# Optimization experiments

Hardware: AMD Instinct MI355X
Metric: run time of the kernel (lower is better)

## Reference

```python
import jax, jax.numpy as jnp
import numpy as np
from jax import lax

INPUT_SIZE, HIDDEN, LAYERS, OUT = 49, 32, 2, 10
B, T = 512, 1024


def _param(key, shape, fan):
    bound = 1.0 / np.sqrt(fan)
    return jax.random.uniform(key, shape, jnp.float32, -bound, bound)


def setup_inputs() -> dict:
    key = jax.random.key(0)
    ks = jax.random.split(key, 12)
    return {
        "x": jax.random.normal(ks[0], (B, T, INPUT_SIZE), jnp.float32),
        "W_ih0": _param(ks[1], (4 * HIDDEN, INPUT_SIZE), HIDDEN),
        "W_hh0": _param(ks[2], (4 * HIDDEN, HIDDEN), HIDDEN),
        "b_ih0": _param(ks[3], (4 * HIDDEN,), HIDDEN),
        "b_hh0": _param(ks[4], (4 * HIDDEN,), HIDDEN),
        "W_ih1": _param(ks[5], (4 * HIDDEN, HIDDEN), HIDDEN),
        "W_hh1": _param(ks[6], (4 * HIDDEN, HIDDEN), HIDDEN),
        "b_ih1": _param(ks[7], (4 * HIDDEN,), HIDDEN),
        "b_hh1": _param(ks[8], (4 * HIDDEN,), HIDDEN),
        "W_out": _param(ks[9], (OUT, HIDDEN), HIDDEN),
        "b_out": _param(ks[10], (OUT,), HIDDEN),
    }


def _lstm_layer(x_tbd, W_ih, W_hh, b_ih, b_hh):
    # x_tbd: [T, B, D]; PyTorch gate order i, f, g, o stacked along 4H.
    H = W_hh.shape[1]
    # Precompute input contribution for all timesteps in one GEMM.
    xg = jnp.einsum('tbd,gd->tbg', x_tbd, W_ih) + b_ih + b_hh  # [T, B, 4H]

    def step(carry, xg_t):
        h, c = carry
        gates = xg_t + h @ W_hh.T  # [B, 4H]
        i, f, g, o = jnp.split(gates, 4, axis=-1)
        i = jax.nn.sigmoid(i)
        f = jax.nn.sigmoid(f)
        g = jnp.tanh(g)
        o = jax.nn.sigmoid(o)
        c = f * c + i * g
        h = o * jnp.tanh(c)
        return (h, c), h

    Bsz = x_tbd.shape[1]
    init = (jnp.zeros((Bsz, H), x_tbd.dtype), jnp.zeros((Bsz, H), x_tbd.dtype))
    _, hs = lax.scan(step, init, xg)
    return hs  # [T, B, H]


def reference(x, W_ih0, W_hh0, b_ih0, b_hh0, W_ih1, W_hh1, b_ih1, b_hh1, W_out, b_out):
    # Eval-mode forward (inter-layer dropout disabled).
    xt = jnp.transpose(x, (1, 0, 2))  # [T, B, 49]
    h0 = _lstm_layer(xt, W_ih0, W_hh0, b_ih0, b_hh0)  # [T, B, 32]
    h1 = _lstm_layer(h0, W_ih1, W_hh1, b_ih1, b_hh1)  # [T, B, 32]
    r_out = jnp.transpose(h1, (1, 0, 2))  # [B, T, 32]
    return r_out @ W_out.T + b_out  # [B, T, 10]
```

## Files before the change

### kernel.cpp

```cpp
#include <hip/hip_runtime.h>
#include <cstddef>

#define TSTEPS 1024
#define NIN    49
#define HID    32
#define OUTD   10
#define XSTR   52
#define NGRP   256
#define RMASK  31

typedef float v2f __attribute__((ext_vector_type(2)));

template<int CTRL>
__device__ __forceinline__ float quad(float v) {
    return __int_as_float(__builtin_amdgcn_mov_dpp(__float_as_int(v), CTRL, 0xF, 0xF, true));
}
__device__ __forceinline__ float sigm(float x) {
    return __builtin_amdgcn_rcpf(1.f + __expf(-x));
}
__device__ __forceinline__ void pkfma(v2f& acc, v2f a, v2f b) {
    asm("v_pk_fma_f32 %0, %1, %2, %0" : "+v"(acc) : "v"(a), "v"(b));
}

__device__ __forceinline__ int ldacq(const int* p) {
    return __hip_atomic_load(p, __ATOMIC_ACQUIRE, __HIP_MEMORY_SCOPE_WORKGROUP);
}
__device__ __forceinline__ void pub(int* p, int v, int lane) {
    if (lane == 0)
        __hip_atomic_store(p, v, __ATOMIC_RELEASE, __HIP_MEMORY_SCOPE_WORKGROUP);
}
__device__ __forceinline__ void waitge(const int* p, int need, int& cache) {
    if (cache >= need) return;
    int c = ldacq(p);
    while (c < need) { __builtin_amdgcn_s_sleep(1); c = ldacq(p); }
    cache = c;
}

#define LOADH2(BASE, H2)                                                     \
    v2f H2[8];                                                               \
    {                                                                        \
        const float4* hp_ = (const float4*)(BASE);                           \
        const float4 a_ = hp_[0], b_ = hp_[1], c_ = hp_[2], d_ = hp_[3];     \
        H2[0] = (v2f){a_.x, a_.y}; H2[1] = (v2f){a_.z, a_.w};                \
        H2[2] = (v2f){b_.x, b_.y}; H2[3] = (v2f){b_.z, b_.w};                \
        H2[4] = (v2f){c_.x, c_.y}; H2[5] = (v2f){c_.z, c_.w};                \
        H2[6] = (v2f){d_.x, d_.y}; H2[7] = (v2f){d_.z, d_.w};                \
    }

#define DOTPK(W2, H2, S0, S1, S2, S3)                                        \
    float S0, S1, S2, S3;                                                    \
    {                                                                        \
        v2f p0 = {0.f,0.f}, p1 = {0.f,0.f}, p2 = {0.f,0.f}, p3 = {0.f,0.f}; \
        _Pragma("unroll")                                                    \
        for (int m_ = 0; m_ < 8; ++m_) {                                     \
            pkfma(p0, W2[0][m_], H2[m_]);                                    \
            pkfma(p1, W2[1][m_], H2[m_]);                                    \
            pkfma(p2, W2[2][m_], H2[m_]);                                    \
            pkfma(p3, W2[3][m_], H2[m_]);                                    \
        }                                                                    \
        S0 = p0.x + p0.y; S1 = p1.x + p1.y;                                  \
        S2 = p2.x + p2.y; S3 = p3.x + p3.y;                                  \
        S0 += quad<0xB1>(S0); S1 += quad<0xB1>(S1);                          \
        S2 += quad<0xB1>(S2); S3 += quad<0xB1>(S3);                          \
    }

__device__ __forceinline__ float gate_act(float s0, float s1, float s2, float s3,
                                          int gp, float& c) {
    const float inA = gp ? s2 + s2 : s0;
    const float inB = gp ? s3 : s1;
    const float sA = sigm(inA);
    const float sB = sigm(inB);
    const float vA = gp ? fmaf(2.f, sA, -1.f) : sA;
    const float xA = quad<0xB1>(vA);
    const float xB = quad<0xB1>(sB);
    const float fg = gp ? xB : sB;
    const float og = gp ? sB : xB;
    c = fmaf(fg, c, vA * xA);
    return og * fmaf(2.f, sigm(c + c), -1.f);
}

extern "C" __global__ void __launch_bounds__(256, 2)
lstm_amort(const float* __restrict__ x,
           const float* __restrict__ Wih0, const float* __restrict__ Whh0,
           const float* __restrict__ bih0, const float* __restrict__ bhh0,
           const float* __restrict__ Wih1, const float* __restrict__ Whh1,
           const float* __restrict__ bih1, const float* __restrict__ bhh1,
           const float* __restrict__ Wout, const float* __restrict__ bout,
           float* __restrict__ y)
{
    const int tid  = threadIdx.x;
    const int lane = tid & 63;
    const int p    = (blockIdx.x ^ (blockIdx.x >> 8)) & 1;
    const int role = (tid >> 6) ^ p;

    __shared__ __align__(16) float xs[2 * 16 * XSTR];
    __shared__ __align__(16) float xg0[32][HID][4];
    __shared__ __align__(16) float xg1[32][HID][4];
    __shared__ __align__(16) float h0r[32][HID];
    __shared__ __align__(16) float h1r[32][HID];
    __shared__ int ctr[5];

    {
        float* z0 = &h0r[0][0];
        float* z1 = &h1r[0][0];
        for (int i = tid; i < 32 * HID; i += 256) { z0[i] = 0.f; z1[i] = 0.f; }
        if (tid < 5) ctr[tid] = -1;
    }
    __syncthreads();

    const float* __restrict__ xb = x + (size_t)blockIdx.x * TSTEPS * NIN;
    float* __restrict__ yb       = y + (size_t)blockIdx.x * TSTEPS * OUTD;

    if (role == 0) {
        const int j = lane >> 1, gp = lane & 1;
        v2f wh0[4][8];
#pragma unroll
        for (int g = 0; g < 4; ++g) {
            const float* wr = Whh0 + (g * HID + j) * HID + 16 * gp;
#pragma unroll
            for (int m = 0; m < 8; ++m) wh0[g][m] = (v2f){wr[2*m], wr[2*m + 1]};
        }
        float c0 = 0.f;
        int cProd = -1, cQd = -1;
        __builtin_amdgcn_s_setprio(1);
        for (int g = 0; g < NGRP; ++g) {
            if ((g & 3) == 0) {
                waitge(&ctr[0], 4 * g + 15, cProd);
                if (g >= 8) waitge(&ctr[2], 4 * g - 17, cQd);
            }
#pragma unroll
            for (int u = 0; u < 4; ++u) {
                const int t = 4 * g + u;
                LOADH2(&h0r[(t + RMASK) & RMASK][16 * gp], hv)
                DOTPK(wh0, hv, s0, s1, s2, s3)
                const float4 xg = *(const float4*)&xg0[t & RMASK][j][0];
                const float hval = gate_act(s0 + xg.x, s1 + xg.y,
                                            s2 + xg.z, s3 + xg.w, gp, c0);
                if (gp == 0) h0r[t & RMASK][j] = hval;
            }
            pub(&ctr[1], 4 * g + 3, lane);
        }
    } else if (role == 1) {
        const int j = lane >> 1, gp = lane & 1;
        v2f wi1[4][8];
        float b1v[4];
#pragma unroll
        for (int g = 0; g < 4; ++g) {
            const float* wr = Wih1 + (g * HID + j) * HID + 16 * gp;
#pragma unroll
            for (int m = 0; m < 8; ++m) wi1[g][m] = (v2f){wr[2*m], wr[2*m + 1]};
            b1v[g] = bih1[g * HID + j] + bhh1[g * HID + j];
        }
        float wo[8], bo = 0.f;
        const int po = lane >> 2, kq = lane & 3;
        if (lane < 40) {
#pragma unroll
            for (int m = 0; m < 8; ++m) wo[m] = Wout[po * HID + kq * 8 + m];
            bo = bout[po];
        } else {
#pragma unroll
            for (int m = 0; m < 8; ++m) wo[m] = 0.f;
        }
        int cL0 = -1, cL1 = -1;
        for (int g = 0; g < NGRP; ++g) {
            if ((g & 3) == 0) {
                waitge(&ctr[1], 4 * g + 15, cL0);
                if (g >= 8) waitge(&ctr[3], 4 * g - 17, cL1);
            }
#pragma unroll
            for (int u = 0; u < 4; ++u) {
                const int t = 4 * g + u;
                LOADH2(&h0r[t & RMASK][16 * gp], hq)
                DOTPK(wi1, hq, q0, q1, q2, q3)
                if (gp == 0) {
                    float4 o;
                    o.x = q0 + b1v[0]; o.y = q1 + b1v[1];
                    o.z = q2 + b1v[2]; o.w = q3 + b1v[3];
                    *(float4*)&xg1[t & RMASK][j][0] = o;
                }
            }
            pub(&ctr[2], 4 * g + 3, lane);
            if (g >= 8) {
                const int gy = g - 8;
#pragma unroll
                for (int u = 0; u < 4; ++u) {
                    const int ty = 4 * gy + u;
                    const float* hb = &h1r[ty & RMASK][kq * 8];
                    const float4 va = *(const float4*)hb;
                    const float4 vb = *(const float4*)(hb + 4);
                    float acc = wo[0]*va.x + wo[1]*va.y + wo[2]*va.z + wo[3]*va.w
                              + wo[4]*vb.x + wo[5]*vb.y + wo[6]*vb.z + wo[7]*vb.w;
                    acc += quad<0xB1>(acc);
                    acc += quad<0x4E>(acc);
                    if (lane < 40 && kq == 0) yb[(size_t)ty * OUTD + po] = acc + bo;
                }
                pub(&ctr[4], 4 * gy + 3, lane);
            }
        }
        for (int gy = NGRP - 8; gy < NGRP; ++gy) {
            waitge(&ctr[3], 4 * gy + 3, cL1);
#pragma unroll
            for (int u = 0; u < 4; ++u) {
                const int ty = 4 * gy + u;
                const float* hb = &h1r[ty & RMASK][kq * 8];
                const float4 va = *(const float4*)hb;
                const float4 vb = *(const float4*)(hb + 4);
                float acc = wo[0]*va.x + wo[1]*va.y + wo[2]*va.z + wo[3]*va.w
                          + wo[4]*vb.x + wo[5]*vb.y + wo[6]*vb.z + wo[7]*vb.w;
                acc += quad<0xB1>(acc);
                acc += quad<0x4E>(acc);
                if (lane < 40 && kq == 0) yb[(size_t)ty * OUTD + po] = acc + bo;
            }
            pub(&ctr[4], 4 * gy + 3, lane);
        }
    } else if (role == 2) {
        const int j = lane >> 1, gp = lane & 1;
        v2f wh1[4][8];
#pragma unroll
        for (int g = 0; g < 4; ++g) {
            const float* wr = Whh1 + (g * HID + j) * HID + 16 * gp;
#pragma unroll
            for (int m = 0; m < 8; ++m) wh1[g][m] = (v2f){wr[2*m], wr[2*m + 1]};
        }
        float c1 = 0.f;
        int cQd = -1, cPrj = -1;
        __builtin_amdgcn_s_setprio(1);
        for (int g = 0; g < NGRP; ++g) {
            if ((g & 3) == 0) {
                waitge(&ctr[2], 4 * g + 15, cQd);
                if (g >= 8) waitge(&ctr[4], 4 * g - 17, cPrj);
            }
#pragma unroll
            for (int u = 0; u < 4; ++u) {
                const int t = 4 * g + u;
                LOADH2(&h1r[(t + RMASK) & RMASK][16 * gp], hv)
                DOTPK(wh1, hv, s0, s1, s2, s3)
                const float4 xg = *(const float4*)&xg1[t & RMASK][j][0];
                const float hval = gate_act(s0 + xg.x, s1 + xg.y,
                                            s2 + xg.z, s3 + xg.w, gp, c1);
                if (gp == 0) h1r[t & RMASK][j] = hval;
            }
            pub(&ctr[3], 4 * g + 3, lane);
        }
    } else {
        const int jj = lane & 31;
        const int gA = lane >> 5;
        const int gB = 2 + (lane >> 5);

        v2f wa2[24], wb2[24];
        float wa48, wb48, b0a, b0b;
        {
            const float* wra = Wih0 + (gA * HID + jj) * NIN;
            const float* wrb = Wih0 + (gB * HID + jj) * NIN;
#pragma unroll
            for (int m = 0; m < 24; ++m) {
                wa2[m] = (v2f){wra[2*m], wra[2*m + 1]};
                wb2[m] = (v2f){wrb[2*m], wrb[2*m + 1]};
            }
            wa48 = wra[48]; wb48 = wrb[48];
            b0a = bih0[gA * HID + jj] + bhh0[gA * HID + jj];
            b0b = bih0[gB * HID + jj] + bhh0[gB * HID + jj];
        }

        int laddr[13];
#pragma unroll
        for (int r = 0; r < 13; ++r) {
            const int idx = lane + r * 64;
            const int s_  = idx / NIN;
            laddr[r] = s_ * XSTR + (idx - s_ * NIN);
        }
        float xr[13];

        auto issue = [&](int cn) {
            const float* src = xb + (size_t)cn * 16 * NIN;
#pragma unroll
            for (int r = 0; r < 12; ++r) xr[r] = src[lane + r * 64];
            if (lane < 16) xr[12] = src[lane + 768];
        };
        auto drain = [&](int cn) {
            float* dst = &xs[(cn & 1) * (16 * XSTR)];
#pragma unroll
            for (int r = 0; r < 12; ++r) dst[laddr[r]] = xr[r];
            if (lane < 16) dst[laddr[12]] = xr[12];
        };
        auto pdot = [&](int t) {
            const float* xp = &xs[((t >> 4) & 1) * (16 * XSTR) + (t & 15) * XSTR];
            const float4* x4 = (const float4*)xp;
            v2f aA0 = (v2f){b0a, 0.f}, aA1 = (v2f){0.f, 0.f};
            v2f aB0 = (v2f){b0b, 0.f}, aB1 = (v2f){0.f, 0.f};
#pragma unroll
            for (int u = 0; u < 12; ++u) {
                const float4 xv = x4[u];
                const v2f xlo = (v2f){xv.x, xv.y};
                const v2f xhi = (v2f){xv.z, xv.w};
                pkfma(aA0, wa2[2*u],     xlo);
                pkfma(aA1, wa2[2*u + 1], xhi);
                pkfma(aB0, wb2[2*u],     xlo);
                pkfma(aB1, wb2[2*u + 1], xhi);
            }
            const float x48 = xp[48];
            const float a0 = fmaf(wa48, x48, (aA0.x + aA0.y) + (aA1.x + aA1.y));
            const float a2 = fmaf(wb48, x48, (aB0.x + aB0.y) + (aB1.x + aB1.y));
            xg0[t & RMASK][jj][gA] = a0;
            xg0[t & RMASK][jj][gB] = a2;
        };

        issue(0);
        drain(0);

        int cL0 = -1;
        for (int g = 0; g < NGRP; ++g) {
            if ((g & 3) == 0 && g >= 8)
                waitge(&ctr[1], 4 * g - 17, cL0);
            const int cn = (g >> 2) + 1;
            if ((g & 3) == 0 && cn < 64) issue(cn);
            pdot(4 * g); pdot(4 * g + 1); pdot(4 * g + 2); pdot(4 * g + 3);
            if ((g & 3) == 2 && cn < 64) drain(cn);
            pub(&ctr[0], 4 * g + 3, lane);
        }
    }
}

extern "C" void kernel_launch(void* const* d_in, const int* in_sizes, int n_in,
                              void* d_out, int out_size, void* d_ws, size_t ws_size,
                              hipStream_t stream) {
    (void)in_sizes; (void)n_in; (void)d_ws; (void)ws_size; (void)out_size;
    const float* x    = (const float*)d_in[0];
    const float* Wih0 = (const float*)d_in[1];
    const float* Whh0 = (const float*)d_in[2];
    const float* bih0 = (const float*)d_in[3];
    const float* bhh0 = (const float*)d_in[4];
    const float* Wih1 = (const float*)d_in[5];
    const float* Whh1 = (const float*)d_in[6];
    const float* bih1 = (const float*)d_in[7];
    const float* bhh1 = (const float*)d_in[8];
    const float* Wout = (const float*)d_in[9];
    const float* bout = (const float*)d_in[10];
    float* y = (float*)d_out;

    lstm_amort<<<dim3(512), dim3(256), 0, stream>>>(
        x, Wih0, Whh0, bih0, bhh0, Wih1, Whh1, bih1, bhh1, Wout, bout, y);
}
```

Baseline: 395.5 us.

## Pack two batch sequences per workgroup and shrink ring buffers to sixteen steps

Each 512-thread workgroup now runs two independent sequences, each with its own four role wavefronts and its own counters, instead of one sequence per 256-thread block. The LDS ring buffers shrink from 32 to 16 timesteps and the producer/consumer waits tighten, so wavefronts poll every two groups instead of four. The goal is to cut LDS per sequence and change how wavefronts are co-scheduled on a CU. The cost is less slack between pipeline stages, more frequent synchronisation, and a launch bound that forces one block per CU.

```diff
diff --git a/kernel.cpp b/kernel.cpp
--- a/kernel.cpp
+++ b/kernel.cpp
@@ -7,7 +7,8 @@
 #define OUTD   10
 #define XSTR   52
 #define NGRP   256
-#define RMASK  31
+#define RMASK  15
+#define NB     2
 
 typedef float v2f __attribute__((ext_vector_type(2)));
 
@@ -79,8 +80,8 @@
     return og * fmaf(2.f, sigm(c + c), -1.f);
 }
 
-extern "C" __global__ void __launch_bounds__(256, 2)
-lstm_amort(const float* __restrict__ x,
+extern "C" __global__ void __launch_bounds__(512, 1)
+lstm_pair8(const float* __restrict__ x,
            const float* __restrict__ Wih0, const float* __restrict__ Whh0,
            const float* __restrict__ bih0, const float* __restrict__ bhh0,
            const float* __restrict__ Wih1, const float* __restrict__ Whh1,
@@ -90,26 +91,28 @@
 {
     const int tid  = threadIdx.x;
     const int lane = tid & 63;
-    const int p    = (blockIdx.x ^ (blockIdx.x >> 8)) & 1;
-    const int role = (tid >> 6) ^ p;
-
-    __shared__ __align__(16) float xs[2 * 16 * XSTR];
-    __shared__ __align__(16) float xg0[32][HID][4];
-    __shared__ __align__(16) float xg1[32][HID][4];
-    __shared__ __align__(16) float h0r[32][HID];
-    __shared__ __align__(16) float h1r[32][HID];
-    __shared__ int ctr[5];
+    const int w    = tid >> 6;
+    const int bi   = w >> 2;
+    const int role = (w & 3) ^ bi;
+
+    __shared__ __align__(16) float xs[NB][2 * 16 * XSTR];
+    __shared__ __align__(16) float xg0[NB][16][HID][4];
+    __shared__ __align__(16) float xg1[NB][16][HID][4];
+    __shared__ __align__(16) float h0r[NB][16][HID];
+    __shared__ __align__(16) float h1r[NB][16][HID];
+    __shared__ int ctr[NB][5];
 
     {
-        float* z0 = &h0r[0][0];
-        float* z1 = &h1r[0][0];
-        for (int i = tid; i < 32 * HID; i += 256) { z0[i] = 0.f; z1[i] = 0.f; }
-        if (tid < 5) ctr[tid] = -1;
+        float* z0 = &h0r[0][0][0];
+        float* z1 = &h1r[0][0][0];
+        for (int i = tid; i < NB * 16 * HID; i += 512) { z0[i] = 0.f; z1[i] = 0.f; }
+        if (tid < NB * 5) ctr[tid / 5][tid % 5] = -1;
     }
     __syncthreads();
 
-    const float* __restrict__ xb = x + (size_t)blockIdx.x * TSTEPS * NIN;
-    float* __restrict__ yb       = y + (size_t)blockIdx.x * TSTEPS * OUTD;
+    const float* __restrict__ xb = x + ((size_t)blockIdx.x * NB + bi) * TSTEPS * NIN;
+    float* __restrict__ yb       = y + ((size_t)blockIdx.x * NB + bi) * TSTEPS * OUTD;
+    int* cr = &ctr[bi][0];
 
     if (role == 0) {
         const int j = lane >> 1, gp = lane & 1;
@@ -124,21 +127,21 @@
         int cProd = -1, cQd = -1;
         __builtin_amdgcn_s_setprio(1);
         for (int g = 0; g < NGRP; ++g) {
-            if ((g & 3) == 0) {
-                waitge(&ctr[0], 4 * g + 15, cProd);
-                if (g >= 8) waitge(&ctr[2], 4 * g - 17, cQd);
+            if ((g & 1) == 0) {
+                waitge(&cr[0], 4 * g + 7, cProd);
+                if (g >= 4) waitge(&cr[2], 4 * g - 9, cQd);
             }
 #pragma unroll
             for (int u = 0; u < 4; ++u) {
                 const int t = 4 * g + u;
-                LOADH2(&h0r[(t + RMASK) & RMASK][16 * gp], hv)
+                LOADH2(&h0r[bi][(t + RMASK) & RMASK][16 * gp], hv)
                 DOTPK(wh0, hv, s0, s1, s2, s3)
-                const float4 xg = *(const float4*)&xg0[t & RMASK][j][0];
+                const float4 xg = *(const float4*)&xg0[bi][t & RMASK][j][0];
                 const float hval = gate_act(s0 + xg.x, s1 + xg.y,
                                             s2 + xg.z, s3 + xg.w, gp, c0);
-                if (gp == 0) h0r[t & RMASK][j] = hval;
-            }
-            pub(&ctr[1], 4 * g + 3, lane);
+                if (gp == 0) h0r[bi][t & RMASK][j] = hval;
+            }
+            pub(&cr[1], 4 * g + 3, lane);
         }
     } else if (role == 1) {
         const int j = lane >> 1, gp = lane & 1;
@@ -163,29 +166,29 @@
         }
         int cL0 = -1, cL1 = -1;
         for (int g = 0; g < NGRP; ++g) {
-            if ((g & 3) == 0) {
-                waitge(&ctr[1], 4 * g + 15, cL0);
-                if (g >= 8) waitge(&ctr[3], 4 * g - 17, cL1);
+            if ((g & 1) == 0) {
+                waitge(&cr[1], 4 * g + 7, cL0);
+                if (g >= 4) waitge(&cr[3], 4 * g - 9, cL1);
             }
 #pragma unroll
             for (int u = 0; u < 4; ++u) {
                 const int t = 4 * g + u;
-                LOADH2(&h0r[t & RMASK][16 * gp], hq)
+                LOADH2(&h0r[bi][t & RMASK][16 * gp], hq)
                 DOTPK(wi1, hq, q0, q1, q2, q3)
                 if (gp == 0) {
                     float4 o;
                     o.x = q0 + b1v[0]; o.y = q1 + b1v[1];
                     o.z = q2 + b1v[2]; o.w = q3 + b1v[3];
-                    *(float4*)&xg1[t & RMASK][j][0] = o;
+                    *(float4*)&xg1[bi][t & RMASK][j][0] = o;
                 }
             }
-            pub(&ctr[2], 4 * g + 3, lane);
-            if (g >= 8) {
-                const int gy = g - 8;
+            pub(&cr[2], 4 * g + 3, lane);
+            if (g >= 4) {
+                const int gy = g - 4;
 #pragma unroll
                 for (int u = 0; u < 4; ++u) {
                     const int ty = 4 * gy + u;
-                    const float* hb = &h1r[ty & RMASK][kq * 8];
+                    const float* hb = &h1r[bi][ty & RMASK][kq * 8];
                     const float4 va = *(const float4*)hb;
                     const float4 vb = *(const float4*)(hb + 4);
                     float acc = wo[0]*va.x + wo[1]*va.y + wo[2]*va.z + wo[3]*va.w
@@ -194,15 +197,15 @@
                     acc += quad<0x4E>(acc);
                     if (lane < 40 && kq == 0) yb[(size_t)ty * OUTD + po] = acc + bo;
                 }
-                pub(&ctr[4], 4 * gy + 3, lane);
-            }
-        }
-        for (int gy = NGRP - 8; gy < NGRP; ++gy) {
-            waitge(&ctr[3], 4 * gy + 3, cL1);
+                pub(&cr[4], 4 * gy + 3, lane);
+            }
+        }
+        for (int gy = NGRP - 4; gy < NGRP; ++gy) {
+            waitge(&cr[3], 4 * gy + 3, cL1);
 #pragma unroll
             for (int u = 0; u < 4; ++u) {
                 const int ty = 4 * gy + u;
-                const float* hb = &h1r[ty & RMASK][kq * 8];
+                const float* hb = &h1r[bi][ty & RMASK][kq * 8];
                 const float4 va = *(const float4*)hb;
                 const float4 vb = *(const float4*)(hb + 4);
                 float acc = wo[0]*va.x + wo[1]*va.y + wo[2]*va.z + wo[3]*va.w
@@ -211,7 +214,7 @@
                 acc += quad<0x4E>(acc);
                 if (lane < 40 && kq == 0) yb[(size_t)ty * OUTD + po] = acc + bo;
             }
-            pub(&ctr[4], 4 * gy + 3, lane);
+            pub(&cr[4], 4 * gy + 3, lane);
         }
     } else if (role == 2) {
         const int j = lane >> 1, gp = lane & 1;
@@ -226,21 +229,21 @@
         int cQd = -1, cPrj = -1;
         __builtin_amdgcn_s_setprio(1);
         for (int g = 0; g < NGRP; ++g) {
-            if ((g & 3) == 0) {
-                waitge(&ctr[2], 4 * g + 15, cQd);
-                if (g >= 8) waitge(&ctr[4], 4 * g - 17, cPrj);
+            if ((g & 1) == 0) {
+                waitge(&cr[2], 4 * g + 7, cQd);
+                if (g >= 4) waitge(&cr[4], 4 * g - 9, cPrj);
             }
 #pragma unroll
             for (int u = 0; u < 4; ++u) {
                 const int t = 4 * g + u;
-                LOADH2(&h1r[(t + RMASK) & RMASK][16 * gp], hv)
+                LOADH2(&h1r[bi][(t + RMASK) & RMASK][16 * gp], hv)
                 DOTPK(wh1, hv, s0, s1, s2, s3)
-                const float4 xg = *(const float4*)&xg1[t & RMASK][j][0];
+                const float4 xg = *(const float4*)&xg1[bi][t & RMASK][j][0];
                 const float hval = gate_act(s0 + xg.x, s1 + xg.y,
                                             s2 + xg.z, s3 + xg.w, gp, c1);
-                if (gp == 0) h1r[t & RMASK][j] = hval;
-            }
-            pub(&ctr[3], 4 * g + 3, lane);
+                if (gp == 0) h1r[bi][t & RMASK][j] = hval;
+            }
+            pub(&cr[3], 4 * g + 3, lane);
         }
     } else {
         const int jj = lane & 31;
@@ -278,13 +281,13 @@
             if (lane < 16) xr[12] = src[lane + 768];
         };
         auto drain = [&](int cn) {
-            float* dst = &xs[(cn & 1) * (16 * XSTR)];
+            float* dst = &xs[bi][(cn & 1) * (16 * XSTR)];
 #pragma unroll
             for (int r = 0; r < 12; ++r) dst[laddr[r]] = xr[r];
             if (lane < 16) dst[laddr[12]] = xr[12];
         };
         auto pdot = [&](int t) {
-            const float* xp = &xs[((t >> 4) & 1) * (16 * XSTR) + (t & 15) * XSTR];
+            const float* xp = &xs[bi][((t >> 4) & 1) * (16 * XSTR) + (t & 15) * XSTR];
             const float4* x4 = (const float4*)xp;
             v2f aA0 = (v2f){b0a, 0.f}, aA1 = (v2f){0.f, 0.f};
             v2f aB0 = (v2f){b0b, 0.f}, aB1 = (v2f){0.f, 0.f};
@@ -301,8 +304,8 @@
             const float x48 = xp[48];
             const float a0 = fmaf(wa48, x48, (aA0.x + aA0.y) + (aA1.x + aA1.y));
             const float a2 = fmaf(wb48, x48, (aB0.x + aB0.y) + (aB1.x + aB1.y));
-            xg0[t & RMASK][jj][gA] = a0;
-            xg0[t & RMASK][jj][gB] = a2;
+            xg0[bi][t & RMASK][jj][gA] = a0;
+            xg0[bi][t & RMASK][jj][gB] = a2;
         };
 
         issue(0);
@@ -310,13 +313,13 @@
 
         int cL0 = -1;
         for (int g = 0; g < NGRP; ++g) {
-            if ((g & 3) == 0 && g >= 8)
-                waitge(&ctr[1], 4 * g - 17, cL0);
+            if ((g & 1) == 0 && g >= 4)
+                waitge(&cr[1], 4 * g - 9, cL0);
             const int cn = (g >> 2) + 1;
             if ((g & 3) == 0 && cn < 64) issue(cn);
             pdot(4 * g); pdot(4 * g + 1); pdot(4 * g + 2); pdot(4 * g + 3);
             if ((g & 3) == 2 && cn < 64) drain(cn);
-            pub(&ctr[0], 4 * g + 3, lane);
+            pub(&cr[0], 4 * g + 3, lane);
         }
     }
 }
@@ -338,6 +341,6 @@
     const float* bout = (const float*)d_in[10];
     float* y = (float*)d_out;
 
-    lstm_amort<<<dim3(512), dim3(256), 0, stream>>>(
+    lstm_pair8<<<dim3(512 / NB), dim3(512), 0, stream>>>(
         x, Wih0, Whh0, bih0, bhh0, Wih1, Whh1, bih1, bhh1, Wout, bout, y);
 }
```

New measurement: 400.6 us. About the same (+1.3%).

## Keep recurrent hidden state in SGPRs via readlane broadcast instead of LDS

Applied to the files above, without the earlier changes.

The two recurrent roles stop reading the previous hidden state from LDS each step. Each lane now holds full 32-wide rows for two gates and multiplies them against a scalar-register copy of h gathered with readlane, using v_pk_fma with SGPR operands. The gate-input loads for four timesteps are also hoisted ahead of the inner loop. This removes an LDS round trip and the cross-lane reduction from the serial critical path, but adds 32 readlane operations per step and a longer FMA chain per lane.

```diff
diff --git a/kernel.cpp b/kernel.cpp
--- a/kernel.cpp
+++ b/kernel.cpp
@@ -1,5 +1,6 @@
 #include <hip/hip_runtime.h>
 #include <cstddef>
+#include <cstdint>
 
 #define TSTEPS 1024
 #define NIN    49
@@ -20,6 +21,9 @@
 }
 __device__ __forceinline__ void pkfma(v2f& acc, v2f a, v2f b) {
     asm("v_pk_fma_f32 %0, %1, %2, %0" : "+v"(acc) : "v"(a), "v"(b));
+}
+__device__ __forceinline__ void pkfma_s(v2f& acc, v2f a, unsigned long long h) {
+    asm("v_pk_fma_f32 %0, %1, %2, %0" : "+v"(acc) : "v"(a), "s"(h));
 }
 
 __device__ __forceinline__ int ldacq(const int* p) {
@@ -79,14 +83,45 @@
     return og * fmaf(2.f, sigm(c + c), -1.f);
 }
 
+#define CHAIN_STEP(WA, WB, HS, XG, GH, CC, HVAL)                             \
+    float HVAL;                                                              \
+    {                                                                        \
+        v2f aP={0.f,0.f}, aQ={0.f,0.f}, bP={0.f,0.f}, bQ={0.f,0.f};          \
+        _Pragma("unroll")                                                    \
+        for (int m_ = 0; m_ < 8; ++m_) {                                     \
+            pkfma_s(aP, WA[m_],     HS[m_]);                                 \
+            pkfma_s(bP, WB[m_],     HS[m_]);                                 \
+            pkfma_s(aQ, WA[8 + m_], HS[8 + m_]);                             \
+            pkfma_s(bQ, WB[8 + m_], HS[8 + m_]);                             \
+        }                                                                    \
+        const float tPa = aP.x + aP.y, tQa = aQ.x + aQ.y;                    \
+        const float tPb = bP.x + bP.y, tQb = bQ.x + bQ.y;                    \
+        const float SA = (GH) ? (tQa + tPa) : (tPa + tQa);                   \
+        const float SB = (GH) ? (tQb + tPb) : (tPb + tQb);                   \
+        const float xa = (GH) ? (XG).z : (XG).x;                             \
+        const float xb = (GH) ? (XG).w : (XG).y;                             \
+        HVAL = gate_act(SA + xa, SB + xb, SA + xa, SB + xb, (GH), CC);       \
+    }
+
+#define GATHER_H(HS, HVAL)                                                   \
+    {                                                                        \
+        const int hb_ = __float_as_int(HVAL);                                \
+        _Pragma("unroll")                                                    \
+        for (int p_ = 0; p_ < 16; ++p_) {                                    \
+            const unsigned lo_ = (unsigned)__builtin_amdgcn_readlane(hb_, 4*p_);     \
+            const unsigned hi_ = (unsigned)__builtin_amdgcn_readlane(hb_, 4*p_ + 2); \
+            HS[p_] = (unsigned long long)lo_ | ((unsigned long long)hi_ << 32);      \
+        }                                                                    \
+    }
+
 extern "C" __global__ void __launch_bounds__(256, 2)
-lstm_amort(const float* __restrict__ x,
-           const float* __restrict__ Wih0, const float* __restrict__ Whh0,
-           const float* __restrict__ bih0, const float* __restrict__ bhh0,
-           const float* __restrict__ Wih1, const float* __restrict__ Whh1,
-           const float* __restrict__ bih1, const float* __restrict__ bhh1,
-           const float* __restrict__ Wout, const float* __restrict__ bout,
-           float* __restrict__ y)
+lstm_sgpr(const float* __restrict__ x,
+          const float* __restrict__ Wih0, const float* __restrict__ Whh0,
+          const float* __restrict__ bih0, const float* __restrict__ bhh0,
+          const float* __restrict__ Wih1, const float* __restrict__ Whh1,
+          const float* __restrict__ bih1, const float* __restrict__ bhh1,
+          const float* __restrict__ Wout, const float* __restrict__ bout,
+          float* __restrict__ y)
 {
     const int tid  = threadIdx.x;
     const int lane = tid & 63;
@@ -112,14 +147,22 @@
     float* __restrict__ yb       = y + (size_t)blockIdx.x * TSTEPS * OUTD;
 
     if (role == 0) {
-        const int j = lane >> 1, gp = lane & 1;
-        v2f wh0[4][8];
-#pragma unroll
-        for (int g = 0; g < 4; ++g) {
-            const float* wr = Whh0 + (g * HID + j) * HID + 16 * gp;
-#pragma unroll
-            for (int m = 0; m < 8; ++m) wh0[g][m] = (v2f){wr[2*m], wr[2*m + 1]};
-        }
+        const int j = lane >> 1, gh = lane & 1;
+        const int gA = 2 * gh, gB = 2 * gh + 1;
+        v2f wA[16], wB[16];
+        {
+            const float* ra = Whh0 + (gA * HID + j) * HID;
+            const float* rb = Whh0 + (gB * HID + j) * HID;
+#pragma unroll
+            for (int m = 0; m < 16; ++m) {
+                wA[m] = (v2f){ra[2*m], ra[2*m + 1]};
+                wB[m] = (v2f){rb[2*m], rb[2*m + 1]};
+            }
+        }
+        unsigned long long hs[16];
+#pragma unroll
+        for (int m = 0; m < 16; ++m) hs[m] = 0ull;
+
         float c0 = 0.f;
         int cProd = -1, cQd = -1;
         __builtin_amdgcn_s_setprio(1);
@@ -128,15 +171,16 @@
                 waitge(&ctr[0], 4 * g + 15, cProd);
                 if (g >= 8) waitge(&ctr[2], 4 * g - 17, cQd);
             }
+            float4 xgf[4];
+#pragma unroll
+            for (int u = 0; u < 4; ++u)
+                xgf[u] = *(const float4*)&xg0[(4 * g + u) & RMASK][j][0];
 #pragma unroll
             for (int u = 0; u < 4; ++u) {
                 const int t = 4 * g + u;
-                LOADH2(&h0r[(t + RMASK) & RMASK][16 * gp], hv)
-                DOTPK(wh0, hv, s0, s1, s2, s3)
-                const float4 xg = *(const float4*)&xg0[t & RMASK][j][0];
-                const float hval = gate_act(s0 + xg.x, s1 + xg.y,
-                                            s2 + xg.z, s3 + xg.w, gp, c0);
-                if (gp == 0) h0r[t & RMASK][j] = hval;
+                CHAIN_STEP(wA, wB, hs, xgf[u], gh, c0, hval)
+                if (gh == 0) h0r[t & RMASK][j] = hval;
+                GATHER_H(hs, hval)
             }
             pub(&ctr[1], 4 * g + 3, lane);
         }
@@ -214,14 +258,22 @@
             pub(&ctr[4], 4 * gy + 3, lane);
         }
     } else if (role == 2) {
-        const int j = lane >> 1, gp = lane & 1;
-        v2f wh1[4][8];
-#pragma unroll
-        for (int g = 0; g < 4; ++g) {
-            const float* wr = Whh1 + (g * HID + j) * HID + 16 * gp;
-#pragma unroll
-            for (int m = 0; m < 8; ++m) wh1[g][m] = (v2f){wr[2*m], wr[2*m + 1]};
-        }
+        const int j = lane >> 1, gh = lane & 1;
+        const int gA = 2 * gh, gB = 2 * gh + 1;
+        v2f wA[16], wB[16];
+        {
+            const float* ra = Whh1 + (gA * HID + j) * HID;
+            const float* rb = Whh1 + (gB * HID + j) * HID;
+#pragma unroll
+            for (int m = 0; m < 16; ++m) {
+                wA[m] = (v2f){ra[2*m], ra[2*m + 1]};
+                wB[m] = (v2f){rb[2*m], rb[2*m + 1]};
+            }
+        }
+        unsigned long long hs[16];
+#pragma unroll
+        for (int m = 0; m < 16; ++m) hs[m] = 0ull;
+
         float c1 = 0.f;
         int cQd = -1, cPrj = -1;
         __builtin_amdgcn_s_setprio(1);
@@ -230,15 +282,16 @@
                 waitge(&ctr[2], 4 * g + 15, cQd);
                 if (g >= 8) waitge(&ctr[4], 4 * g - 17, cPrj);
             }
+            float4 xgf[4];
+#pragma unroll
+            for (int u = 0; u < 4; ++u)
+                xgf[u] = *(const float4*)&xg1[(4 * g + u) & RMASK][j][0];
 #pragma unroll
             for (int u = 0; u < 4; ++u) {
                 const int t = 4 * g + u;
-                LOADH2(&h1r[(t + RMASK) & RMASK][16 * gp], hv)
-                DOTPK(wh1, hv, s0, s1, s2, s3)
-                const float4 xg = *(const float4*)&xg1[t & RMASK][j][0];
-                const float hval = gate_act(s0 + xg.x, s1 + xg.y,
-                                            s2 + xg.z, s3 + xg.w, gp, c1);
-                if (gp == 0) h1r[t & RMASK][j] = hval;
+                CHAIN_STEP(wA, wB, hs, xgf[u], gh, c1, hval)
+                if (gh == 0) h1r[t & RMASK][j] = hval;
+                GATHER_H(hs, hval)
             }
             pub(&ctr[3], 4 * g + 3, lane);
         }
@@ -338,6 +391,6 @@
     const float* bout = (const float*)d_in[10];
     float* y = (float*)d_out;
 
-    lstm_amort<<<dim3(512), dim3(256), 0, stream>>>(
+    lstm_sgpr<<<dim3(512), dim3(256), 0, stream>>>(
         x, Wih0, Whh0, bih0, bhh0, Wih1, Whh1, bih1, bhh1, Wout, bout, y);
 }
```

New measurement: 474.1 us. 1.2x slower.
